# Kernel tuning notes

Measured on AMD Instinct MI355X. Metric: run time of the kernel, lower is better.

## Reference

```python
import jax, jax.numpy as jnp
import numpy as np

B, T, I, H, L, HPR = 256, 512, 128, 256, 64, 50


def _mlp(x, W1, b1, W2, b2):
    # Linear -> ReLU -> Linear, torch convention y = x @ W.T + b
    return jax.nn.relu(x @ W1.T + b1) @ W2.T + b2


def setup_inputs() -> dict:
    key = jax.random.key(0)
    ks = jax.random.split(key, 16)
    s = 0.05
    return {
        "x": jax.random.uniform(ks[0], (B, T, I), dtype=jnp.float32),
        "hidden": jnp.zeros((B, H), jnp.float32),
        "noise": jax.random.normal(ks[1], (B, T, L), dtype=jnp.float32),
        "Wpm1": s * jax.random.normal(ks[2], (HPR, H)), "bpm1": jnp.zeros((HPR,)),
        "Wpm2": s * jax.random.normal(ks[3], (L, HPR)), "bpm2": jnp.zeros((L,)),
        "Wpl1": s * jax.random.normal(ks[4], (HPR, H)), "bpl1": jnp.zeros((HPR,)),
        "Wpl2": s * jax.random.normal(ks[5], (L, HPR)), "bpl2": jnp.zeros((L,)),
        "Wqm1": s * jax.random.normal(ks[6], (HPR, I + H)), "bqm1": jnp.zeros((HPR,)),
        "Wqm2": s * jax.random.normal(ks[7], (L, HPR)), "bqm2": jnp.zeros((L,)),
        "Wql1": s * jax.random.normal(ks[8], (HPR, I + H)), "bql1": jnp.zeros((HPR,)),
        "Wql2": s * jax.random.normal(ks[9], (L, HPR)), "bql2": jnp.zeros((L,)),
        "Wh1": s * jax.random.normal(ks[10], (HPR, I + H + L)), "bh1": jnp.zeros((HPR,)),
        "Wh2": s * jax.random.normal(ks[11], (H, HPR)), "bh2": jnp.zeros((H,)),
        "Wo": s * jax.random.normal(ks[12], (I, H + L)), "bo": jnp.zeros((I,)),
    }


def reference(x, hidden, noise,
              Wpm1, bpm1, Wpm2, bpm2, Wpl1, bpl1, Wpl2, bpl2,
              Wqm1, bqm1, Wqm2, bqm2, Wql1, bql1, Wql2, bql2,
              Wh1, bh1, Wh2, bh2, Wo, bo):
    def step(h, inp):
        x_t, eps = inp  # [B,I], [B,L]
        xh = jnp.concatenate([x_t, h], axis=1)
        q_mu = _mlp(xh, Wqm1, bqm1, Wqm2, bqm2)
        q_lv = _mlp(xh, Wql1, bql1, Wql2, bql2)
        p_mu = _mlp(h, Wpm1, bpm1, Wpm2, bpm2)
        p_lv = _mlp(h, Wpl1, bpl1, Wpl2, bpl2)
        z = q_mu + jnp.exp(0.5 * q_lv) * eps
        h_next = _mlp(jnp.concatenate([x_t, h, z], axis=1), Wh1, bh1, Wh2, bh2)
        out = jax.nn.sigmoid(jnp.concatenate([h, z], axis=1) @ Wo.T + bo)
        return h_next, (out, p_mu, p_lv, q_mu, q_lv)

    xs = (jnp.swapaxes(x, 0, 1), jnp.swapaxes(noise, 0, 1))  # [T,B,*]
    _, (x_hat, p_mu, p_lv, q_mu, q_lv) = jax.lax.scan(step, hidden, xs)
    tb = lambda a: jnp.swapaxes(a, 0, 1)  # [T,B,*] -> [B,T,*]
    return tb(x_hat), tb(p_mu), tb(p_lv), tb(q_mu), tb(q_lv)
```

## Files before the change

kernel.cpp:

```cpp
#include <hip/hip_runtime.h>
#include <stdint.h>


typedef _Float16 f16x2 __attribute__((ext_vector_type(2)));

__device__ __forceinline__ float bf2f(uint16_t u) {
  union { uint32_t u; float f; } c; c.u = ((uint32_t)u) << 16; return c.f;
}
__device__ __forceinline__ uint16_t f2bf(float f) {
  union { float f; uint32_t u; } c; c.f = f;
  uint32_t u = c.u;
  uint32_t r = (u + 0x7FFFu + ((u >> 16) & 1u)) >> 16;
  return (uint16_t)r;
}
__device__ __forceinline__ uint32_t packh2(float a, float b) {
  union { f16x2 h; uint32_t u; } c;
  c.h.x = (_Float16)a; c.h.y = (_Float16)b; return c.u;
}
__device__ __forceinline__ float fdot2(uint32_t a, uint32_t b, float c) {
  union { uint32_t u; f16x2 h; } ua, ub; ua.u = a; ub.u = b;
#if __has_builtin(__builtin_amdgcn_fdot2)
  return __builtin_amdgcn_fdot2(ua.h, ub.h, c, false);
#else
  return c + (float)ua.h.x * (float)ub.h.x + (float)ua.h.y * (float)ub.h.y;
#endif
}

__device__ __forceinline__ int sniff_bf16(const uint32_t* xw) {
  int cnt = 0;
#pragma unroll
  for (int i = 0; i < 64; ++i) {
    uint32_t e = (xw[i] >> 7) & 0xFFu;
    cnt += (e >= 0x70u && e <= 0x7Fu) ? 1 : 0;
  }
  return cnt >= 32;
}
__device__ __forceinline__ float loadIn(const void* p, size_t i, int isbf) {
  return isbf ? bf2f(((const uint16_t*)p)[i]) : ((const float*)p)[i];
}
__device__ __forceinline__ void storeOut(void* p, size_t i, float v, int isbf) {
  if (isbf) ((uint16_t*)p)[i] = f2bf(v);
  else      ((float*)p)[i] = v;
}

#define WS_W2   75776
#define WS_BIAS 88832
#define N_JOBS  89792

struct PrepArgs {
  const void* W[11];
  const void* B[11];
  const uint32_t* xw;
};

__global__ void vrnn_prep(PrepArgs a, uint32_t* __restrict__ ws) {
  const int isbf = sniff_bf16(a.xw);
  int j = blockIdx.x * 256 + threadIdx.x;
  if (j < 75776) {
    int p = j >> 9, tid = j & 511;
    const void* W; int row, k, K; bool valid;
    if (p < 48)       { W = a.W[p < 24 ? 0 : 1]; int pj = (p < 24) ? p : p - 24;
                        row = tid >> 3; k = (tid & 7) * 48 + pj * 2; K = 384; valid = row < 50; }
    else if (p < 80)  { W = a.W[p < 64 ? 2 : 3]; int pj = (p < 64) ? p - 48 : p - 64;
                        row = tid >> 3; k = (tid & 7) * 32 + pj * 2; K = 256; valid = row < 50; }
    else if (p < 108) { W = a.W[4]; row = tid >> 3; k = (tid & 7) * 56 + (p - 80) * 2; K = 448; valid = row < 50; }
    else              { W = a.W[5]; row = tid >> 2; k = (tid & 3) * 80 + (p - 108) * 2; K = 320; valid = true; }
    float f0 = valid ? loadIn(W, (size_t)row * K + k, isbf)     : 0.f;
    float f1 = valid ? loadIn(W, (size_t)row * K + k + 1, isbf) : 0.f;
    ws[j] = packh2(f0, f1);
  } else if (j < WS_BIAS) {
    int q = j - WS_W2;
    if (q < 6400) {
      int m = q / 1600, rem = q % 1600, r = rem / 25, kp = rem % 25, k = kp * 2;
      ws[j] = packh2(loadIn(a.W[6 + m], r * 50 + k, isbf),
                     loadIn(a.W[6 + m], r * 50 + k + 1, isbf));
    } else {
      int rem = q - 6400, r = rem / 26, kp = rem % 26, k = kp * 2;
      float f0 = (k     < 50) ? loadIn(a.W[10], r * 50 + k,     isbf) : 0.f;
      float f1 = (k + 1 < 50) ? loadIn(a.W[10], r * 50 + k + 1, isbf) : 0.f;
      ws[j] = packh2(f0, f1);
    }
  } else if (j < N_JOBS) {
    int q = j - WS_BIAS; float v = 0.f;
    if (q < 320)      { int m = q >> 6, i = q & 63; if (i < 50) v = loadIn(a.B[m], i, isbf); }
    else if (q < 576) { int m = (q - 320) >> 6;     v = loadIn(a.B[5 + m], q & 63, isbf); }
    else if (q < 832) { v = loadIn(a.B[9],  q - 576, isbf); }
    else              { v = loadIn(a.B[10], q - 832, isbf); }
    ((float*)ws)[j] = v;
  }
}

__global__ __launch_bounds__(512, 2) void vrnn_main(
    const void* __restrict__ x, const void* __restrict__ hidden,
    const void* __restrict__ noise, const uint32_t* __restrict__ ws,
    void* __restrict__ out)
{
  __shared__ uint32_t s_w2[13056];
  __shared__ float    s_bias[960];
  __shared__ __align__(16) _Float16 s_v[448];
  __shared__ __align__(8)  _Float16 s_act[320];
  __shared__ float    s_xhat[128];

  const int tid = threadIdx.x;
  const int b = blockIdx.x;
  const int isbf = sniff_bf16((const uint32_t*)x);

  uint32_t wqm1[24], wql1[24], wpm1[16], wpl1[16], wh1[28], wo[40];
#pragma unroll
  for (int i = 0; i < 24; ++i) wqm1[i] = ws[(0   + i) * 512 + tid];
#pragma unroll
  for (int i = 0; i < 24; ++i) wql1[i] = ws[(24  + i) * 512 + tid];
#pragma unroll
  for (int i = 0; i < 16; ++i) wpm1[i] = ws[(48  + i) * 512 + tid];
#pragma unroll
  for (int i = 0; i < 16; ++i) wpl1[i] = ws[(64  + i) * 512 + tid];
#pragma unroll
  for (int i = 0; i < 28; ++i) wh1[i]  = ws[(80  + i) * 512 + tid];
#pragma unroll
  for (int i = 0; i < 40; ++i) wo[i]   = ws[(108 + i) * 512 + tid];

  for (int i = tid; i < 13056; i += 512) s_w2[i] = ws[WS_W2 + i];
  {
    const float* wsf = (const float*)(ws + WS_BIAS);
    for (int i = tid; i < 960; i += 512) s_bias[i] = wsf[i];
  }

  if (tid < 128)      s_v[tid] = (_Float16)loadIn(x, (size_t)b * 65536 + tid, isbf);
  else if (tid < 384) s_v[tid] = (_Float16)loadIn(hidden, (size_t)b * 256 + (tid - 128), isbf);
  else if (tid < 448) s_v[tid] = (_Float16)0.f;

  float eps_r = 0.f;
  if (tid < 64) eps_r = loadIn(noise, (size_t)b * 32768 + tid, isbf);
  float xnext = 0.f;

  const int row8 = tid >> 3, c8 = tid & 7;
  const int row4 = tid >> 2, c4 = tid & 3;
  const int rh = tid >> 1, ch = tid & 1;
  const uint4* v4 = (const uint4*)s_v;

  __syncthreads();

  const size_t OFF_PMU = 16777216u;
  const size_t OFF_PLV = 25165824u;
  const size_t OFF_QMU = 33554432u;
  const size_t OFF_QLV = 41943040u;

#pragma unroll 1
  for (int t = 0; t < 512; ++t) {
    const size_t bt = (size_t)b * 512 + t;
    if (tid >= 384) {
      int tn = (t < 511) ? t + 1 : 511;
      xnext = loadIn(x, ((size_t)b * 512 + tn) * 128 + (tid - 384), isbf);
    }

    float a_qm = 0.f, a_ql = 0.f, a_pm = 0.f, a_pl = 0.f;
    {
      const int g = c8 * 6;
#pragma unroll
      for (int i = 0; i < 6; ++i) {
        uint4 q = v4[g + i];
        a_qm = fdot2(wqm1[4*i+0], q.x, a_qm); a_ql = fdot2(wql1[4*i+0], q.x, a_ql);
        a_qm = fdot2(wqm1[4*i+1], q.y, a_qm); a_ql = fdot2(wql1[4*i+1], q.y, a_ql);
        a_qm = fdot2(wqm1[4*i+2], q.z, a_qm); a_ql = fdot2(wql1[4*i+2], q.z, a_ql);
        a_qm = fdot2(wqm1[4*i+3], q.w, a_qm); a_ql = fdot2(wql1[4*i+3], q.w, a_ql);
      }
      const int g2 = 16 + c8 * 4;
#pragma unroll
      for (int i = 0; i < 4; ++i) {
        uint4 q = v4[g2 + i];
        a_pm = fdot2(wpm1[4*i+0], q.x, a_pm); a_pl = fdot2(wpl1[4*i+0], q.x, a_pl);
        a_pm = fdot2(wpm1[4*i+1], q.y, a_pm); a_pl = fdot2(wpl1[4*i+1], q.y, a_pl);
        a_pm = fdot2(wpm1[4*i+2], q.z, a_pm); a_pl = fdot2(wpl1[4*i+2], q.z, a_pl);
        a_pm = fdot2(wpm1[4*i+3], q.w, a_pm); a_pl = fdot2(wpl1[4*i+3], q.w, a_pl);
      }
    }
#pragma unroll
    for (int m = 1; m < 8; m <<= 1) {
      a_qm += __shfl_xor(a_qm, m);
      a_ql += __shfl_xor(a_ql, m);
      a_pm += __shfl_xor(a_pm, m);
      a_pl += __shfl_xor(a_pl, m);
    }
    if (c8 == 0) {
      s_act[row8]       = (_Float16)fmaxf(a_qm + s_bias[row8],       0.f);
      s_act[64 + row8]  = (_Float16)fmaxf(a_ql + s_bias[64 + row8],  0.f);
      s_act[128 + row8] = (_Float16)fmaxf(a_pm + s_bias[128 + row8], 0.f);
      s_act[192 + row8] = (_Float16)fmaxf(a_pl + s_bias[192 + row8], 0.f);
    }
    __syncthreads();

    if (tid < 128) {
      const int r = tid & 63;
      const bool isq = tid < 64;
      const uint32_t* Wm = s_w2 + (isq ? 0 : 3200) + r * 25;
      const uint32_t* Wl = s_w2 + (isq ? 1600 : 4800) + r * 25;
      const uint32_t* am = (const uint32_t*)(s_act + (isq ? 0 : 128));
      const uint32_t* al = (const uint32_t*)(s_act + (isq ? 64 : 192));
      float mu = s_bias[(isq ? 320 : 448) + r];
      float lv = s_bias[(isq ? 384 : 512) + r];
#pragma unroll
      for (int kp = 0; kp < 25; ++kp) {
        mu = fdot2(Wm[kp], am[kp], mu);
        lv = fdot2(Wl[kp], al[kp], lv);
      }
      storeOut(out, (isq ? OFF_QMU : OFF_PMU) + bt * 64 + r, mu, isbf);
      storeOut(out, (isq ? OFF_QLV : OFF_PLV) + bt * 64 + r, lv, isbf);
      if (isq) {
        float z = mu + __expf(0.5f * lv) * eps_r;
        s_v[384 + r] = (_Float16)z;
        int tn = (t < 511) ? t + 1 : 511;
        eps_r = loadIn(noise, ((size_t)b * 512 + tn) * 64 + r, isbf);
      }
    }
    __syncthreads();

    float a_o = 0.f, a_h = 0.f;
    {
      const int g = 16 + c4 * 10;
#pragma unroll
      for (int i = 0; i < 10; ++i) {
        uint4 q = v4[g + i];
        a_o = fdot2(wo[4*i+0], q.x, a_o);
        a_o = fdot2(wo[4*i+1], q.y, a_o);
        a_o = fdot2(wo[4*i+2], q.z, a_o);
        a_o = fdot2(wo[4*i+3], q.w, a_o);
      }
      const int g2 = c8 * 7;
#pragma unroll
      for (int i = 0; i < 7; ++i) {
        uint4 q = v4[g2 + i];
        a_h = fdot2(wh1[4*i+0], q.x, a_h);
        a_h = fdot2(wh1[4*i+1], q.y, a_h);
        a_h = fdot2(wh1[4*i+2], q.z, a_h);
        a_h = fdot2(wh1[4*i+3], q.w, a_h);
      }
    }
    a_o += __shfl_xor(a_o, 1); a_o += __shfl_xor(a_o, 2);
    a_h += __shfl_xor(a_h, 1); a_h += __shfl_xor(a_h, 2); a_h += __shfl_xor(a_h, 4);
    if (c4 == 0) s_xhat[row4] = 1.f / (1.f + __expf(-(a_o + s_bias[832 + row4])));
    if (c8 == 0) s_act[256 + row8] = (_Float16)fmaxf(a_h + s_bias[256 + row8], 0.f);
    __syncthreads();

    {
      const uint32_t* ahp = (const uint32_t*)(s_act + 256);
      const uint32_t* Wr = s_w2 + 6400 + rh * 26 + ch * 13;
      float hh = 0.f;
#pragma unroll
      for (int kp = 0; kp < 13; ++kp) hh = fdot2(Wr[kp], ahp[ch * 13 + kp], hh);
      hh += __shfl_xor(hh, 1);
      if (ch == 0) s_v[128 + rh] = (_Float16)(hh + s_bias[576 + rh]);
    }
    if (tid >= 256 && tid < 384) storeOut(out, bt * 128 + (tid - 256), s_xhat[tid - 256], isbf);
    if (tid >= 384) s_v[tid - 384] = (_Float16)xnext;
    __syncthreads();
  }
}

extern "C" void kernel_launch(void* const* d_in, const int* in_sizes, int n_in,
                              void* d_out, int out_size, void* d_ws, size_t ws_size,
                              hipStream_t stream) {
  (void)in_sizes; (void)n_in; (void)out_size; (void)ws_size;
  PrepArgs a;
  a.W[0]  = d_in[11];
  a.W[1]  = d_in[15];
  a.W[2]  = d_in[3];
  a.W[3]  = d_in[7];
  a.W[4]  = d_in[19];
  a.W[5]  = d_in[23];
  a.W[6]  = d_in[13];
  a.W[7]  = d_in[17];
  a.W[8]  = d_in[5];
  a.W[9]  = d_in[9];
  a.W[10] = d_in[21];
  a.B[0]  = d_in[12];
  a.B[1]  = d_in[16];
  a.B[2]  = d_in[4];
  a.B[3]  = d_in[8];
  a.B[4]  = d_in[20];
  a.B[5]  = d_in[14];
  a.B[6]  = d_in[18];
  a.B[7]  = d_in[6];
  a.B[8]  = d_in[10];
  a.B[9]  = d_in[22];
  a.B[10] = d_in[24];
  a.xw    = (const uint32_t*)d_in[0];

  uint32_t* ws = (uint32_t*)d_ws;
  vrnn_prep<<<dim3((N_JOBS + 255) / 256), dim3(256), 0, stream>>>(a, ws);
  vrnn_main<<<dim3(256), dim3(512), 0, stream>>>(d_in[0], d_in[1], d_in[2], ws, d_out);
}
```

Measured before the change: 1.513 ms.

## Hoist x,h parts of Wh1 and Wo dots ahead of z, spread layer-2 across threads

```diff
diff --git a/kernel.cpp b/kernel.cpp
--- a/kernel.cpp
+++ b/kernel.cpp
@@ -26,6 +26,31 @@
 #endif
 }
 
+template <int CTRL>
+__device__ __forceinline__ float dpp_mov(float x) {
+#if __has_builtin(__builtin_amdgcn_update_dpp)
+  union { float f; int i; } a, b;
+  a.f = x;
+  b.i = __builtin_amdgcn_update_dpp(0, a.i, CTRL, 0xF, 0xF, true);
+  return b.f;
+#else
+  return __shfl_xor(x, (CTRL == 0xB1) ? 1 : (CTRL == 0x4E) ? 2 : 4);
+#endif
+}
+__device__ __forceinline__ float red2(float x) {
+  return x + dpp_mov<0xB1>(x);
+}
+__device__ __forceinline__ float red4(float x) {
+  x += dpp_mov<0xB1>(x); x += dpp_mov<0x4E>(x); return x;
+}
+__device__ __forceinline__ float red8(float x) {
+  x += dpp_mov<0xB1>(x); x += dpp_mov<0x4E>(x); x += dpp_mov<0x141>(x); return x;
+}
+
+__device__ __forceinline__ void barrier_lds() {
+  asm volatile("s_waitcnt lgkmcnt(0)\n\ts_barrier" ::: "memory");
+}
+
 __device__ __forceinline__ int sniff_bf16(const uint32_t* xw) {
   int cnt = 0;
 #pragma unroll
@@ -44,8 +69,8 @@
 }
 
 #define WS_W2   75776
-#define WS_BIAS 88832
-#define N_JOBS  89792
+#define WS_BIAS 94208
+#define N_JOBS  95168
 
 struct PrepArgs {
   const void* W[11];
@@ -58,28 +83,30 @@
   int j = blockIdx.x * 256 + threadIdx.x;
   if (j < 75776) {
     int p = j >> 9, tid = j & 511;
+    int t8 = tid >> 3, c8 = tid & 7;
     const void* W; int row, k, K; bool valid;
-    if (p < 48)       { W = a.W[p < 24 ? 0 : 1]; int pj = (p < 24) ? p : p - 24;
-                        row = tid >> 3; k = (tid & 7) * 48 + pj * 2; K = 384; valid = row < 50; }
-    else if (p < 80)  { W = a.W[p < 64 ? 2 : 3]; int pj = (p < 64) ? p - 48 : p - 64;
-                        row = tid >> 3; k = (tid & 7) * 32 + pj * 2; K = 256; valid = row < 50; }
-    else if (p < 108) { W = a.W[4]; row = tid >> 3; k = (tid & 7) * 56 + (p - 80) * 2; K = 448; valid = row < 50; }
-    else              { W = a.W[5]; row = tid >> 2; k = (tid & 3) * 80 + (p - 108) * 2; K = 320; valid = true; }
+    if (p < 24)       { W = a.W[0]; row = t8; k = c8*48 + p*2;        K = 384; valid = row < 50; }
+    else if (p < 48)  { W = a.W[1]; row = t8; k = c8*48 + (p-24)*2;   K = 384; valid = row < 50; }
+    else if (p < 64)  { W = a.W[2]; row = t8; k = c8*32 + (p-48)*2;   K = 256; valid = row < 50; }
+    else if (p < 80)  { W = a.W[3]; row = t8; k = c8*32 + (p-64)*2;   K = 256; valid = row < 50; }
+    else if (p < 104) { W = a.W[4]; row = t8; k = c8*48 + (p-80)*2;   K = 448; valid = row < 50; }
+    else if (p < 108) { W = a.W[4]; row = t8; k = 384 + c8*8 + (p-104)*2; K = 448; valid = row < 50; }
+    else if (p < 124) { W = a.W[5]; row = t8;      k = c8*32 + (p-108)*2;     K = 320; valid = true; }
+    else if (p < 128) { W = a.W[5]; row = t8;      k = 256 + c8*8 + (p-124)*2; K = 320; valid = true; }
+    else if (p < 144) { W = a.W[5]; row = 64 + t8; k = c8*32 + (p-128)*2;     K = 320; valid = true; }
+    else              { W = a.W[5]; row = 64 + t8; k = 256 + c8*8 + (p-144)*2; K = 320; valid = true; }
     float f0 = valid ? loadIn(W, (size_t)row * K + k, isbf)     : 0.f;
     float f1 = valid ? loadIn(W, (size_t)row * K + k + 1, isbf) : 0.f;
     ws[j] = packh2(f0, f1);
   } else if (j < WS_BIAS) {
     int q = j - WS_W2;
-    if (q < 6400) {
-      int m = q / 1600, rem = q % 1600, r = rem / 25, kp = rem % 25, k = kp * 2;
-      ws[j] = packh2(loadIn(a.W[6 + m], r * 50 + k, isbf),
-                     loadIn(a.W[6 + m], r * 50 + k + 1, isbf));
-    } else {
-      int rem = q - 6400, r = rem / 26, kp = rem % 26, k = kp * 2;
-      float f0 = (k     < 50) ? loadIn(a.W[10], r * 50 + k,     isbf) : 0.f;
-      float f1 = (k + 1 < 50) ? loadIn(a.W[10], r * 50 + k + 1, isbf) : 0.f;
-      ws[j] = packh2(f0, f1);
-    }
+    const void* W; int r, kp;
+    if (q < 9216) { int m = q / 2304, rem = q % 2304; r = rem / 36; kp = rem % 36; W = a.W[6 + m]; }
+    else          { int rem = q - 9216;               r = rem / 36; kp = rem % 36; W = a.W[10]; }
+    uint32_t v = 0;
+    if (kp < 25) v = packh2(loadIn(W, r * 50 + kp * 2, isbf),
+                            loadIn(W, r * 50 + kp * 2 + 1, isbf));
+    ws[j] = v;
   } else if (j < N_JOBS) {
     int q = j - WS_BIAS; float v = 0.f;
     if (q < 320)      { int m = q >> 6, i = q & 63; if (i < 50) v = loadIn(a.B[m], i, isbf); }
@@ -95,17 +122,18 @@
     const void* __restrict__ noise, const uint32_t* __restrict__ ws,
     void* __restrict__ out)
 {
-  __shared__ uint32_t s_w2[13056];
-  __shared__ float    s_bias[960];
+  __shared__ __align__(16) uint32_t s_w2[18432];
+  __shared__ float s_bias[960];
   __shared__ __align__(16) _Float16 s_v[448];
-  __shared__ __align__(8)  _Float16 s_act[320];
-  __shared__ float    s_xhat[128];
+  __shared__ __align__(16) uint32_t s_actu[180];
+  _Float16* s_act = (_Float16*)s_actu;
 
   const int tid = threadIdx.x;
   const int b = blockIdx.x;
   const int isbf = sniff_bf16((const uint32_t*)x);
 
-  uint32_t wqm1[24], wql1[24], wpm1[16], wpl1[16], wh1[28], wo[40];
+  uint32_t wqm1[24], wql1[24], wpm1[16], wpl1[16];
+  uint32_t wh1a[24], wh1z[4], wo0h[16], wo0z[4], wo1h[16], wo1z[4];
 #pragma unroll
   for (int i = 0; i < 24; ++i) wqm1[i] = ws[(0   + i) * 512 + tid];
 #pragma unroll
@@ -115,11 +143,19 @@
 #pragma unroll
   for (int i = 0; i < 16; ++i) wpl1[i] = ws[(64  + i) * 512 + tid];
 #pragma unroll
-  for (int i = 0; i < 28; ++i) wh1[i]  = ws[(80  + i) * 512 + tid];
-#pragma unroll
-  for (int i = 0; i < 40; ++i) wo[i]   = ws[(108 + i) * 512 + tid];
-
-  for (int i = tid; i < 13056; i += 512) s_w2[i] = ws[WS_W2 + i];
+  for (int i = 0; i < 24; ++i) wh1a[i] = ws[(80  + i) * 512 + tid];
+#pragma unroll
+  for (int i = 0; i < 4;  ++i) wh1z[i] = ws[(104 + i) * 512 + tid];
+#pragma unroll
+  for (int i = 0; i < 16; ++i) wo0h[i] = ws[(108 + i) * 512 + tid];
+#pragma unroll
+  for (int i = 0; i < 4;  ++i) wo0z[i] = ws[(124 + i) * 512 + tid];
+#pragma unroll
+  for (int i = 0; i < 16; ++i) wo1h[i] = ws[(128 + i) * 512 + tid];
+#pragma unroll
+  for (int i = 0; i < 4;  ++i) wo1z[i] = ws[(144 + i) * 512 + tid];
+
+  for (int i = tid; i < 18432; i += 512) s_w2[i] = ws[WS_W2 + i];
   {
     const float* wsf = (const float*)(ws + WS_BIAS);
     for (int i = tid; i < 960; i += 512) s_bias[i] = wsf[i];
@@ -129,14 +165,14 @@
   else if (tid < 384) s_v[tid] = (_Float16)loadIn(hidden, (size_t)b * 256 + (tid - 128), isbf);
   else if (tid < 448) s_v[tid] = (_Float16)0.f;
 
-  float eps_r = 0.f;
-  if (tid < 64) eps_r = loadIn(noise, (size_t)b * 32768 + tid, isbf);
-  float xnext = 0.f;
-
   const int row8 = tid >> 3, c8 = tid & 7;
-  const int row4 = tid >> 2, c4 = tid & 3;
+  const int i2 = tid >> 2, c4 = tid & 3;
   const int rh = tid >> 1, ch = tid & 1;
   const uint4* v4 = (const uint4*)s_v;
+
+  float eps_r = 0.f;
+  if (c4 == 0 && i2 < 64) eps_r = loadIn(noise, (size_t)b * 32768 + i2, isbf);
+  float xnext = 0.f;
 
   __syncthreads();
 
@@ -153,106 +189,119 @@
       xnext = loadIn(x, ((size_t)b * 512 + tn) * 128 + (tid - 384), isbf);
     }
 
-    float a_qm = 0.f, a_ql = 0.f, a_pm = 0.f, a_pl = 0.f;
+    float a_qm = 0.f, a_ql = 0.f, a_hx = 0.f;
     {
       const int g = c8 * 6;
 #pragma unroll
       for (int i = 0; i < 6; ++i) {
         uint4 q = v4[g + i];
-        a_qm = fdot2(wqm1[4*i+0], q.x, a_qm); a_ql = fdot2(wql1[4*i+0], q.x, a_ql);
-        a_qm = fdot2(wqm1[4*i+1], q.y, a_qm); a_ql = fdot2(wql1[4*i+1], q.y, a_ql);
-        a_qm = fdot2(wqm1[4*i+2], q.z, a_qm); a_ql = fdot2(wql1[4*i+2], q.z, a_ql);
-        a_qm = fdot2(wqm1[4*i+3], q.w, a_qm); a_ql = fdot2(wql1[4*i+3], q.w, a_ql);
+        a_qm = fdot2(wqm1[4*i+0], q.x, a_qm); a_ql = fdot2(wql1[4*i+0], q.x, a_ql); a_hx = fdot2(wh1a[4*i+0], q.x, a_hx);
+        a_qm = fdot2(wqm1[4*i+1], q.y, a_qm); a_ql = fdot2(wql1[4*i+1], q.y, a_ql); a_hx = fdot2(wh1a[4*i+1], q.y, a_hx);
+        a_qm = fdot2(wqm1[4*i+2], q.z, a_qm); a_ql = fdot2(wql1[4*i+2], q.z, a_ql); a_hx = fdot2(wh1a[4*i+2], q.z, a_hx);
+        a_qm = fdot2(wqm1[4*i+3], q.w, a_qm); a_ql = fdot2(wql1[4*i+3], q.w, a_ql); a_hx = fdot2(wh1a[4*i+3], q.w, a_hx);
       }
-      const int g2 = 16 + c8 * 4;
+    }
+    float a_pm = 0.f, a_pl = 0.f, a_o0 = 0.f, a_o1 = 0.f;
+    {
+      const int g = 16 + c8 * 4;
 #pragma unroll
       for (int i = 0; i < 4; ++i) {
-        uint4 q = v4[g2 + i];
+        uint4 q = v4[g + i];
         a_pm = fdot2(wpm1[4*i+0], q.x, a_pm); a_pl = fdot2(wpl1[4*i+0], q.x, a_pl);
+        a_o0 = fdot2(wo0h[4*i+0], q.x, a_o0); a_o1 = fdot2(wo1h[4*i+0], q.x, a_o1);
         a_pm = fdot2(wpm1[4*i+1], q.y, a_pm); a_pl = fdot2(wpl1[4*i+1], q.y, a_pl);
+        a_o0 = fdot2(wo0h[4*i+1], q.y, a_o0); a_o1 = fdot2(wo1h[4*i+1], q.y, a_o1);
         a_pm = fdot2(wpm1[4*i+2], q.z, a_pm); a_pl = fdot2(wpl1[4*i+2], q.z, a_pl);
+        a_o0 = fdot2(wo0h[4*i+2], q.z, a_o0); a_o1 = fdot2(wo1h[4*i+2], q.z, a_o1);
         a_pm = fdot2(wpm1[4*i+3], q.w, a_pm); a_pl = fdot2(wpl1[4*i+3], q.w, a_pl);
+        a_o0 = fdot2(wo0h[4*i+3], q.w, a_o0); a_o1 = fdot2(wo1h[4*i+3], q.w, a_o1);
       }
     }
-#pragma unroll
-    for (int m = 1; m < 8; m <<= 1) {
-      a_qm += __shfl_xor(a_qm, m);
-      a_ql += __shfl_xor(a_ql, m);
-      a_pm += __shfl_xor(a_pm, m);
-      a_pl += __shfl_xor(a_pl, m);
-    }
+    a_qm = red8(a_qm); a_ql = red8(a_ql); a_pm = red8(a_pm); a_pl = red8(a_pl);
     if (c8 == 0) {
       s_act[row8]       = (_Float16)fmaxf(a_qm + s_bias[row8],       0.f);
-      s_act[64 + row8]  = (_Float16)fmaxf(a_ql + s_bias[64 + row8],  0.f);
-      s_act[128 + row8] = (_Float16)fmaxf(a_pm + s_bias[128 + row8], 0.f);
-      s_act[192 + row8] = (_Float16)fmaxf(a_pl + s_bias[192 + row8], 0.f);
-    }
-    __syncthreads();
-
-    if (tid < 128) {
-      const int r = tid & 63;
-      const bool isq = tid < 64;
-      const uint32_t* Wm = s_w2 + (isq ? 0 : 3200) + r * 25;
-      const uint32_t* Wl = s_w2 + (isq ? 1600 : 4800) + r * 25;
-      const uint32_t* am = (const uint32_t*)(s_act + (isq ? 0 : 128));
-      const uint32_t* al = (const uint32_t*)(s_act + (isq ? 64 : 192));
-      float mu = s_bias[(isq ? 320 : 448) + r];
-      float lv = s_bias[(isq ? 384 : 512) + r];
-#pragma unroll
-      for (int kp = 0; kp < 25; ++kp) {
-        mu = fdot2(Wm[kp], am[kp], mu);
-        lv = fdot2(Wl[kp], al[kp], lv);
+      s_act[72 + row8]  = (_Float16)fmaxf(a_ql + s_bias[64 + row8],  0.f);
+      s_act[144 + row8] = (_Float16)fmaxf(a_pm + s_bias[128 + row8], 0.f);
+      s_act[216 + row8] = (_Float16)fmaxf(a_pl + s_bias[192 + row8], 0.f);
+    }
+    barrier_lds();
+
+    {
+      const bool isq = i2 < 64;
+      const int r = isq ? i2 : i2 - 64;
+      const uint32_t* Wm = s_w2 + (isq ? 0 : 4608) + r * 36 + c4 * 8;
+      const uint32_t* Wl = s_w2 + (isq ? 2304 : 6912) + r * 36 + c4 * 8;
+      const uint32_t* am = s_actu + (isq ? 0 : 72) + c4 * 8;
+      const uint32_t* al = s_actu + (isq ? 36 : 108) + c4 * 8;
+      uint4 wm0 = *(const uint4*)Wm, wm1 = *(const uint4*)(Wm + 4);
+      uint4 wl0 = *(const uint4*)Wl, wl1 = *(const uint4*)(Wl + 4);
+      uint4 am0 = *(const uint4*)am, am1 = *(const uint4*)(am + 4);
+      uint4 al0 = *(const uint4*)al, al1 = *(const uint4*)(al + 4);
+      float mu0 = 0.f, mu1 = 0.f, lv0 = 0.f, lv1 = 0.f;
+      mu0 = fdot2(wm0.x, am0.x, mu0); lv0 = fdot2(wl0.x, al0.x, lv0);
+      mu1 = fdot2(wm1.x, am1.x, mu1); lv1 = fdot2(wl1.x, al1.x, lv1);
+      mu0 = fdot2(wm0.y, am0.y, mu0); lv0 = fdot2(wl0.y, al0.y, lv0);
+      mu1 = fdot2(wm1.y, am1.y, mu1); lv1 = fdot2(wl1.y, al1.y, lv1);
+      mu0 = fdot2(wm0.z, am0.z, mu0); lv0 = fdot2(wl0.z, al0.z, lv0);
+      mu1 = fdot2(wm1.z, am1.z, mu1); lv1 = fdot2(wl1.z, al1.z, lv1);
+      mu0 = fdot2(wm0.w, am0.w, mu0); lv0 = fdot2(wl0.w, al0.w, lv0);
+      mu1 = fdot2(wm1.w, am1.w, mu1); lv1 = fdot2(wl1.w, al1.w, lv1);
+      float mu = red4(mu0 + mu1);
+      float lv = red4(lv0 + lv1);
+      if (c4 == 0) {
+        mu += s_bias[(isq ? 320 : 448) + r];
+        lv += s_bias[(isq ? 384 : 512) + r];
+        storeOut(out, (isq ? OFF_QMU : OFF_PMU) + bt * 64 + r, mu, isbf);
+        storeOut(out, (isq ? OFF_QLV : OFF_PLV) + bt * 64 + r, lv, isbf);
+        if (isq) {
+          float z = mu + __expf(0.5f * lv) * eps_r;
+          s_v[384 + r] = (_Float16)z;
+          int tn = (t < 511) ? t + 1 : 511;
+          eps_r = loadIn(noise, ((size_t)b * 512 + tn) * 64 + r, isbf);
+        }
       }
-      storeOut(out, (isq ? OFF_QMU : OFF_PMU) + bt * 64 + r, mu, isbf);
-      storeOut(out, (isq ? OFF_QLV : OFF_PLV) + bt * 64 + r, lv, isbf);
-      if (isq) {
-        float z = mu + __expf(0.5f * lv) * eps_r;
-        s_v[384 + r] = (_Float16)z;
-        int tn = (t < 511) ? t + 1 : 511;
-        eps_r = loadIn(noise, ((size_t)b * 512 + tn) * 64 + r, isbf);
+    }
+    barrier_lds();
+
+    {
+      uint4 qz = v4[48 + c8];
+      float ah = a_hx, o0 = a_o0, o1 = a_o1;
+      ah = fdot2(wh1z[0], qz.x, ah); o0 = fdot2(wo0z[0], qz.x, o0); o1 = fdot2(wo1z[0], qz.x, o1);
+      ah = fdot2(wh1z[1], qz.y, ah); o0 = fdot2(wo0z[1], qz.y, o0); o1 = fdot2(wo1z[1], qz.y, o1);
+      ah = fdot2(wh1z[2], qz.z, ah); o0 = fdot2(wo0z[2], qz.z, o0); o1 = fdot2(wo1z[2], qz.z, o1);
+      ah = fdot2(wh1z[3], qz.w, ah); o0 = fdot2(wo0z[3], qz.w, o0); o1 = fdot2(wo1z[3], qz.w, o1);
+      ah = red8(ah); o0 = red8(o0); o1 = red8(o1);
+      if (c8 == 0) {
+        s_act[288 + row8] = (_Float16)fmaxf(ah + s_bias[256 + row8], 0.f);
+        float s0 = 1.f / (1.f + __expf(-(o0 + s_bias[832 + row8])));
+        float s1 = 1.f / (1.f + __expf(-(o1 + s_bias[896 + row8])));
+        storeOut(out, bt * 128 + row8, s0, isbf);
+        storeOut(out, bt * 128 + 64 + row8, s1, isbf);
       }
     }
-    __syncthreads();
-
-    float a_o = 0.f, a_h = 0.f;
-    {
-      const int g = 16 + c4 * 10;
-#pragma unroll
-      for (int i = 0; i < 10; ++i) {
-        uint4 q = v4[g + i];
-        a_o = fdot2(wo[4*i+0], q.x, a_o);
-        a_o = fdot2(wo[4*i+1], q.y, a_o);
-        a_o = fdot2(wo[4*i+2], q.z, a_o);
-        a_o = fdot2(wo[4*i+3], q.w, a_o);
-      }
-      const int g2 = c8 * 7;
-#pragma unroll
-      for (int i = 0; i < 7; ++i) {
-        uint4 q = v4[g2 + i];
-        a_h = fdot2(wh1[4*i+0], q.x, a_h);
-        a_h = fdot2(wh1[4*i+1], q.y, a_h);
-        a_h = fdot2(wh1[4*i+2], q.z, a_h);
-        a_h = fdot2(wh1[4*i+3], q.w, a_h);
-      }
-    }
-    a_o += __shfl_xor(a_o, 1); a_o += __shfl_xor(a_o, 2);
-    a_h += __shfl_xor(a_h, 1); a_h += __shfl_xor(a_h, 2); a_h += __shfl_xor(a_h, 4);
-    if (c4 == 0) s_xhat[row4] = 1.f / (1.f + __expf(-(a_o + s_bias[832 + row4])));
-    if (c8 == 0) s_act[256 + row8] = (_Float16)fmaxf(a_h + s_bias[256 + row8], 0.f);
-    __syncthreads();
-
-    {
-      const uint32_t* ahp = (const uint32_t*)(s_act + 256);
-      const uint32_t* Wr = s_w2 + 6400 + rh * 26 + ch * 13;
-      float hh = 0.f;
-#pragma unroll
-      for (int kp = 0; kp < 13; ++kp) hh = fdot2(Wr[kp], ahp[ch * 13 + kp], hh);
-      hh += __shfl_xor(hh, 1);
+    barrier_lds();
+
+    {
+      const uint32_t* Wr = s_w2 + 9216 + rh * 36 + ch * 16;
+      const uint32_t* ap = s_actu + 144 + ch * 16;
+      uint4 w0 = *(const uint4*)Wr,        w1 = *(const uint4*)(Wr + 4);
+      uint4 w2 = *(const uint4*)(Wr + 8),  w3 = *(const uint4*)(Wr + 12);
+      uint4 a0 = *(const uint4*)ap,        a1 = *(const uint4*)(ap + 4);
+      uint4 a2 = *(const uint4*)(ap + 8),  a3 = *(const uint4*)(ap + 12);
+      float h0 = 0.f, h1 = 0.f;
+      h0 = fdot2(w0.x, a0.x, h0); h1 = fdot2(w2.x, a2.x, h1);
+      h0 = fdot2(w0.y, a0.y, h0); h1 = fdot2(w2.y, a2.y, h1);
+      h0 = fdot2(w0.z, a0.z, h0); h1 = fdot2(w2.z, a2.z, h1);
+      h0 = fdot2(w0.w, a0.w, h0); h1 = fdot2(w2.w, a2.w, h1);
+      h0 = fdot2(w1.x, a1.x, h0); h1 = fdot2(w3.x, a3.x, h1);
+      h0 = fdot2(w1.y, a1.y, h0); h1 = fdot2(w3.y, a3.y, h1);
+      h0 = fdot2(w1.z, a1.z, h0); h1 = fdot2(w3.z, a3.z, h1);
+      h0 = fdot2(w1.w, a1.w, h0); h1 = fdot2(w3.w, a3.w, h1);
+      float hh = red2(h0 + h1);
       if (ch == 0) s_v[128 + rh] = (_Float16)(hh + s_bias[576 + rh]);
     }
-    if (tid >= 256 && tid < 384) storeOut(out, bt * 128 + (tid - 256), s_xhat[tid - 256], isbf);
     if (tid >= 384) s_v[tid - 384] = (_Float16)xnext;
-    __syncthreads();
+    barrier_lds();
   }
 }
 
```

Result: faster. 1.267 ms (-16.2%).
